# Kernel tuning notes

Measured on AMD Instinct MI355X. Metric: run time of the kernel, lower is better.

The kernel has to match this reference:

```python
import jax, jax.numpy as jnp
import numpy as np

B = 1000        # graphs in batch
T_PER = 250     # tasks per graph
M_PER = 50      # machines per graph
N_T = B * T_PER
N_M = B * M_PER
D_T = 16        # INPUT_TASK_DIM
D_M = 8         # INPUT_MACHINE_DIM
H = 128         # hidden_dim
IN_PREV_IDX = 0
TASK_FEAT_IDX = 1
EPS = 1e-5      # BatchNorm eps


def _mk_params(rng):
    def lin(i, o):
        return (rng.standard_normal((i, o)).astype(np.float32) / np.sqrt(i),
                np.zeros(o, np.float32))
    p = {}
    p['bn_t_gamma'] = np.ones(D_T, np.float32); p['bn_t_beta'] = np.zeros(D_T, np.float32)
    p['Wt1'], p['bt1'] = lin(D_T, H); p['Wt2'], p['bt2'] = lin(H, H)
    p['bn_m_gamma'] = np.ones(D_M, np.float32); p['bn_m_beta'] = np.zeros(D_M, np.float32)
    p['Wm1'], p['bm1'] = lin(D_M, H); p['Wm2'], p['bm2'] = lin(H, H)
    p['Wa1'], p['ba1'] = lin(2 * H, H); p['Wa2'], p['ba2'] = lin(H, H)
    p['Wl1'], p['bl1'] = lin(3 * H, H); p['Wl2'], p['bl2'] = lin(H, H)
    p['Wo1'], p['bo1'] = lin(H, H); p['Wo2'], p['bo2'] = lin(H, 1)
    return p


def setup_inputs() -> dict:
    rng = np.random.default_rng(0)
    xt = rng.standard_normal((N_T, D_T)).astype(np.float32)
    # prev-task flag: even task ids are 'prev'
    xt[:, IN_PREV_IDX] = (np.arange(N_T) % 2 == 0).astype(np.float32)
    # per-graph machine assignment in [0, M_PER), or -1 (unassigned) every 10th task
    lm = rng.integers(0, M_PER, N_T)
    lm[np.arange(N_T) % 10 == 0] = -1
    xt[:, TASK_FEAT_IDX] = lm.astype(np.float32)
    xm = rng.standard_normal((N_M, D_M)).astype(np.float32)
    inp = {'x_tasks': jnp.asarray(xt), 'x_machines': jnp.asarray(xm)}
    inp.update({k: jnp.asarray(v) for k, v in _mk_params(rng).items()})
    inp['x_tasks_batch'] = jnp.asarray(np.repeat(np.arange(B), T_PER).astype(np.int32))
    inp['x_machines_batch'] = jnp.asarray(np.repeat(np.arange(B), M_PER).astype(np.int32))
    # labels are tasks 0,5,10,...; prev tasks are even ids -> prev-local index t//2
    # label tasks that are prev: t % 10 == 0 -> prev_tasks_label_idx = 5*arange(N_T//10)
    inp['label_idx'] = jnp.asarray((5 * np.arange(N_T // 10)).astype(np.int32))
    inp['num_graphs'] = B
    return inp


def _bn(x, g, b):
    # BatchNorm1d in training mode: biased batch stats
    mu = x.mean(axis=0)
    var = x.var(axis=0)
    return g * (x - mu) * jax.lax.rsqrt(var + EPS) + b


def _seg_mean(x, seg, n):
    s = jax.ops.segment_sum(x, seg, num_segments=n)
    c = jax.ops.segment_sum(jnp.ones((x.shape[0], 1), x.dtype), seg, num_segments=n)
    return s / jnp.maximum(c, 1.0)


def reference(x_tasks, x_machines, bn_t_gamma, bn_t_beta, Wt1, bt1, Wt2, bt2,
              bn_m_gamma, bn_m_beta, Wm1, bm1, Wm2, bm2,
              Wa1, ba1, Wa2, ba2, Wl1, bl1, Wl2, bl2,
              Wo1, bo1, Wo2, bo2,
              x_tasks_batch, x_machines_batch, label_idx, num_graphs):
    nm = x_machines.shape[0]
    # tasks_select_assignment: local machine id -> global machine row (or pad row nm)
    tm_col = x_tasks[:, TASK_FEAT_IDX]
    cnt_m = jnp.bincount(x_machines_batch, length=num_graphs)
    cum = jnp.cumsum(cnt_m) - cnt_m  # cumulative machines per graph
    task_m = jnp.where(tm_col == -1.0, nm,
                       tm_col.astype(jnp.int32) + cum[x_tasks_batch].astype(jnp.int32))
    # node embeddings: BN -> Linear -> ReLU -> Linear -> ReLU
    th = jax.nn.relu(jax.nn.relu(_bn(x_tasks, bn_t_gamma, bn_t_beta) @ Wt1 + bt1) @ Wt2 + bt2)
    mh = jax.nn.relu(jax.nn.relu(_bn(x_machines, bn_m_gamma, bn_m_beta) @ Wm1 + bm1) @ Wm2 + bm2)
    # global aggregation per graph (scatter_mean) + MLP
    aggr = jnp.concatenate([_seg_mean(th, x_tasks_batch, num_graphs),
                            _seg_mean(mh, x_machines_batch, num_graphs)], axis=1)
    aggr = jax.nn.relu(aggr @ Wa1 + ba1) @ Wa2 + ba2
    # gather machine embedding per task (pad row of zeros for unassigned)
    mh_pad = jnp.concatenate([mh, jnp.zeros((1, H), mh.dtype)], axis=0)
    cat = jnp.concatenate([th, aggr[x_tasks_batch], mh_pad[task_m]], axis=1)  # [N_T, 3H]
    h = jax.nn.relu(cat @ Wl1 + bl1) @ Wl2 + bl2
    out = (jax.nn.relu(h @ Wo1 + bo1) @ Wo2 + bo2)[label_idx]
    return out
```

## Files before the change

### kernel.cpp

```cpp
#include <hip/hip_runtime.h>

constexpr int B     = 1000;
constexpr int T_PER = 250;
constexpr int M_PER = 50;
constexpr int N_T   = B * T_PER;
constexpr int N_M   = B * M_PER;
constexpr int H     = 128;
constexpr int N_LBL = 25000;
constexpr float EPS = 1e-05f;

constexpr int NB_T = 256;
constexpr int NB_M = 64;
constexpr int NB_P = 64;

constexpr int OFF_PART_T = 0;
constexpr int OFF_PART_M = OFF_PART_T + NB_T * 32;
constexpr int OFF_AT     = OFF_PART_M + NB_M * 16;
constexpr int OFF_BT     = OFF_AT + 16;
constexpr int OFF_AM     = OFF_BT + 16;
constexpr int OFF_BM     = OFF_AM + 8;
constexpr int OFF_BT1F   = OFF_BM + 8;
constexpr int OFF_BM1F   = OFF_BT1F + 128;
constexpr int OFF_MEANT  = OFF_BM1F + 128;
constexpr int OFF_MEANM  = OFF_MEANT + B * H;
constexpr int OFF_AGG2   = OFF_MEANM + B * H;
constexpr int OFF_HALF   = OFF_AGG2 + B * H;
constexpr int HO_WT1  = 0;
constexpr int HO_WT2  = 4096;
constexpr int HO_WM1  = 20480;
constexpr int HO_WM2  = 24576;
constexpr int HO_WA1  = 40960;
constexpr int HO_WA2  = 73728;
constexpr int HO_WL1  = 90112;
constexpr int HO_WL2  = 139264;
constexpr int HO_WO1  = 155648;
constexpr int HO_XT16 = 172032;
constexpr int HO_XM16 = HO_XT16 + N_T * 16;

typedef _Float16 f16x8 __attribute__((ext_vector_type(8)));
typedef _Float16 f16x4 __attribute__((ext_vector_type(4)));
typedef float f32x4 __attribute__((ext_vector_type(4)));

#define MFMA16(a, b, c) __builtin_amdgcn_mfma_f32_16x16x32_f16(a, b, c, 0, 0, 0)

template <int C, int NB>
__device__ __forceinline__ void stats_body(const float* __restrict__ x,
                                           _Float16* __restrict__ x16, int nelem,
                                           float* __restrict__ part, int blk, int t,
                                           float* ls, float* lq) {
    float s = 0.f, q = 0.f;
    for (int e = blk * 256 + t; e < nelem; e += NB * 256) {
        float v = x[e];
        s += v;
        q += v * v;
        x16[e] = (_Float16)v;
    }
    ls[t] = s; lq[t] = q;
    __syncthreads();
    if (t < C) {
        float S = 0.f, Q = 0.f;
        for (int u = t; u < 256; u += C) { S += ls[u]; Q += lq[u]; }
        part[blk * 2 * C + t] = S;
        part[blk * 2 * C + C + t] = Q;
    }
}

__device__ __forceinline__ void cvt_tr(const float* __restrict__ src, _Float16* __restrict__ dst,
                                       int K, int Kp, int tid, int nt) {
    for (int idx = tid; idx < 128 * Kp; idx += nt) {
        int c = idx / Kp, k = idx - c * Kp;
        float v = (k < K) ? src[k * 128 + c] : 0.f;
        dst[idx] = (_Float16)v;
    }
}

__global__ __launch_bounds__(256) void stats_prep_kernel(
        const float* __restrict__ xt, const float* __restrict__ xm,
        _Float16* __restrict__ xt16, _Float16* __restrict__ xm16,
        const float* __restrict__ Wt2, const float* __restrict__ Wm2,
        const float* __restrict__ Wa1, const float* __restrict__ Wa2,
        const float* __restrict__ Wl1, const float* __restrict__ Wl2,
        const float* __restrict__ Wo1,
        float* __restrict__ wsf, _Float16* __restrict__ wh) {
    __shared__ float ls[256], lq[256];
    const int bid = blockIdx.x, t = threadIdx.x;
    if (bid < NB_T) {
        stats_body<16, NB_T>(xt, xt16, N_T * 16, wsf + OFF_PART_T, bid, t, ls, lq);
    } else if (bid < NB_T + NB_M) {
        stats_body<8, NB_M>(xm, xm16, N_M * 8, wsf + OFF_PART_M, bid - NB_T, t, ls, lq);
    } else {
        const int tid = (bid - NB_T - NB_M) * 256 + t;
        const int nt = NB_P * 256;
        cvt_tr(Wt2, wh + HO_WT2, 128, 128, tid, nt);
        cvt_tr(Wm2, wh + HO_WM2, 128, 128, tid, nt);
        cvt_tr(Wa1, wh + HO_WA1, 256, 256, tid, nt);
        cvt_tr(Wa2, wh + HO_WA2, 128, 128, tid, nt);
        cvt_tr(Wl1, wh + HO_WL1, 384, 384, tid, nt);
        cvt_tr(Wl2, wh + HO_WL2, 128, 128, tid, nt);
        cvt_tr(Wo1, wh + HO_WO1, 128, 128, tid, nt);
    }
}

__global__ __launch_bounds__(256) void finalize_kernel(
        const float* __restrict__ gt, const float* __restrict__ btb,
        const float* __restrict__ gm, const float* __restrict__ bmb,
        const float* __restrict__ Wt1, const float* __restrict__ bt1,
        const float* __restrict__ Wm1, const float* __restrict__ bm1,
        float* __restrict__ ws, _Float16* __restrict__ wh) {
    __shared__ float red[256];
    __shared__ float statT[32], statM[16];
    __shared__ float shT[16], shM[8];
    __shared__ float saT[16], saM[8];
    const int t = threadIdx.x;
    {
        const int slot = t & 31, chunk = t >> 5;
        const float* p = ws + OFF_PART_T;
        float s = 0.f;
        for (int b = chunk * 32; b < chunk * 32 + 32; b++) s += p[b * 32 + slot];
        red[t] = s;
    }
    __syncthreads();
    if (t < 32) {
        float v = 0.f;
#pragma unroll
        for (int c = 0; c < 8; c++) v += red[t + 32 * c];
        statT[t] = v;
    }
    __syncthreads();
    {
        float s = 0.f;
        if (t < 128) {
            const int slot = t & 15, chunk = t >> 4;
            const float* p = ws + OFF_PART_M;
            for (int b = chunk * 8; b < chunk * 8 + 8; b++) s += p[b * 16 + slot];
        }
        red[t] = s;
    }
    __syncthreads();
    if (t < 16) {
        float v = 0.f;
#pragma unroll
        for (int c = 0; c < 8; c++) v += red[t + 16 * c];
        statM[t] = v;
    }
    __syncthreads();
    if (t < 16) {
        float mu  = statT[t] / (float)N_T;
        float var = statT[16 + t] / (float)N_T - mu * mu;
        float a   = gt[t] * rsqrtf(var + EPS);
        ws[OFF_AT + t] = a;
        float b = btb[t] - mu * a;
        ws[OFF_BT + t] = b;
        shT[t] = b;
        saT[t] = a;
    } else if (t < 24) {
        int c = t - 16;
        float mu  = statM[c] / (float)N_M;
        float var = statM[8 + c] / (float)N_M - mu * mu;
        float a   = gm[c] * rsqrtf(var + EPS);
        ws[OFF_AM + c] = a;
        float b = bmb[c] - mu * a;
        ws[OFF_BM + c] = b;
        shM[c] = b;
        saM[c] = a;
    }
    __syncthreads();
    if (t < 128) {
        float s = bt1[t];
#pragma unroll
        for (int k = 0; k < 16; k++) s += shT[k] * Wt1[k * 128 + t];
        ws[OFF_BT1F + t] = s;
        _Float16 row[32];
#pragma unroll
        for (int k = 0; k < 16; k++) row[k] = (_Float16)(Wt1[k * 128 + t] * saT[k]);
        float bh = (float)(_Float16)s;
        row[16] = (_Float16)s;
        row[17] = (_Float16)(s - bh);
#pragma unroll
        for (int k = 18; k < 32; k++) row[k] = (_Float16)0.f;
#pragma unroll
        for (int q = 0; q < 4; q++)
            *(f16x8*)(wh + HO_WT1 + t * 32 + q * 8) = *(const f16x8*)(row + q * 8);
    } else {
        int c = t - 128;
        float s = bm1[c];
#pragma unroll
        for (int k = 0; k < 8; k++) s += shM[k] * Wm1[k * 128 + c];
        ws[OFF_BM1F + c] = s;
        _Float16 row[32];
#pragma unroll
        for (int k = 0; k < 8; k++) row[k] = (_Float16)(Wm1[k * 128 + c] * saM[k]);
        float bh = (float)(_Float16)s;
        row[8] = (_Float16)s;
        row[9] = (_Float16)(s - bh);
#pragma unroll
        for (int k = 10; k < 32; k++) row[k] = (_Float16)0.f;
#pragma unroll
        for (int q = 0; q < 4; q++)
            *(f16x8*)(wh + HO_WM1 + c * 32 + q * 8) = *(const f16x8*)(row + q * 8);
    }
}

__device__ __forceinline__ void zacc(f32x4 acc[4][2]) {
#pragma unroll
    for (int rg = 0; rg < 4; rg++)
#pragma unroll
        for (int mi = 0; mi < 2; mi++) acc[rg][mi] = (f32x4){0.f, 0.f, 0.f, 0.f};
}

__device__ __forceinline__ void ld32(f16x8 w[2], const _Float16* __restrict__ WT,
                                     int m0, int r, int gq) {
#pragma unroll
    for (int mi = 0; mi < 2; mi++)
        w[mi] = *(const f16x8*)(WT + ((m0 + mi) * 16 + r) * 32 + gq * 8);
}

__device__ __forceinline__ void ld128(f16x8 w[2][4], const _Float16* __restrict__ WT,
                                      int lda, int k0, int m0, int r, int gq) {
#pragma unroll
    for (int mi = 0; mi < 2; mi++)
#pragma unroll
        for (int ks = 0; ks < 4; ks++)
            w[mi][ks] = *(const f16x8*)(WT + ((m0 + mi) * 16 + r) * lda + k0 + ks * 32 + gq * 8);
}

__device__ __forceinline__ void mm32g(const f16x8 w[2], const f16x8 xb[4], f32x4 acc[4][2]) {
#pragma unroll
    for (int rg = 0; rg < 4; rg++) {
        acc[rg][0] = MFMA16(w[0], xb[rg], acc[rg][0]);
        acc[rg][1] = MFMA16(w[1], xb[rg], acc[rg][1]);
    }
}

__device__ __forceinline__ void mm32(const f16x8 w[2], const _Float16* __restrict__ act,
                                     int rstride, int r, int gq, f32x4 acc[4][2]) {
#pragma unroll
    for (int rg = 0; rg < 4; rg++) {
        const f16x8 bf = *(const f16x8*)(act + (rg * 16 + r) * rstride + gq * 8);
        acc[rg][0] = MFMA16(w[0], bf, acc[rg][0]);
        acc[rg][1] = MFMA16(w[1], bf, acc[rg][1]);
    }
}

__device__ __forceinline__ void mm128(const f16x8 w[2][4], const _Float16* __restrict__ act,
                                      int rstride, int r, int gq, f32x4 acc[4][2]) {
#pragma unroll
    for (int rg = 0; rg < 4; rg++)
#pragma unroll
        for (int ks = 0; ks < 4; ks++) {
            const f16x8 bf = *(const f16x8*)(act + (rg * 16 + r) * rstride + ks * 32 + gq * 8);
            acc[rg][0] = MFMA16(w[0][ks], bf, acc[rg][0]);
            acc[rg][1] = MFMA16(w[1][ks], bf, acc[rg][1]);
        }
}

__device__ __forceinline__ void epi_cs(const f32x4 acc[4][2], const f32x4 bv[2],
                                       _Float16* __restrict__ dst, int dstride,
                                       int m0, int r, int gq, bool relu) {
#pragma unroll
    for (int rg = 0; rg < 4; rg++)
#pragma unroll
        for (int mi = 0; mi < 2; mi++) {
            f16x4 hv;
#pragma unroll
            for (int j = 0; j < 4; j++) {
                float v = acc[rg][mi][j] + bv[mi][j];
                if (relu) v = fmaxf(v, 0.f);
                hv[j] = (_Float16)v;
            }
            *(f16x4*)(dst + (rg * 16 + r) * dstride + (m0 + mi) * 16 + gq * 4) = hv;
        }
}

__global__ __launch_bounds__(256, 3) void seg_tile4(
        const _Float16* __restrict__ xt16, const _Float16* __restrict__ xm16,
        const _Float16* __restrict__ wh, const float* __restrict__ wsf,
        const float* __restrict__ bt2, const float* __restrict__ bm2,
        float* __restrict__ meanT, float* __restrict__ meanM) {
    __shared__ __attribute__((aligned(16))) _Float16 h1s[64 * 136];
    const int t = threadIdx.x, lane = t & 63, w = t >> 6;
    const int r = lane & 15, gq = lane >> 4;
    const int m0 = 2 * w;
    const bool taskb = (blockIdx.x < B);
    const _Float16* W1T = wh + (taskb ? HO_WT1 : HO_WM1);
    const _Float16* W2T = wh + (taskb ? HO_WT2 : HO_WM2);
    const float* b1f = wsf + (taskb ? OFF_BT1F : OFF_BM1F);
    const float* b2  = taskb ? bt2 : bm2;
    const _Float16* x16 = taskb ? xt16 : xm16;
    const int ROWS = taskb ? T_PER : M_PER;
    const int CIN  = taskb ? 16 : 8;
    f16x8 w1[2]; ld32(w1, W1T, m0, r, gq);
    f16x8 w2[2][4]; ld128(w2, W2T, 128, 0, m0, r, gq);
    f32x4 b1v[2], b2v[2];
#pragma unroll
    for (int mi = 0; mi < 2; mi++) {
        b1v[mi] = *(const f32x4*)(b1f + (m0 + mi) * 16 + gq * 4);
        b2v[mi] = *(const f32x4*)(b2 + (m0 + mi) * 16 + gq * 4);
    }
    f16x8 z8;
#pragma unroll
    for (int e = 0; e < 8; e++) z8[e] = (_Float16)0.f;
    const bool loader = taskb ? (gq < 2) : (gq == 0);
    const int gb = taskb ? blockIdx.x : 0;
    const int mg0 = taskb ? 0 : (blockIdx.x - B) * 4;
    const f32x4 zf = (f32x4){0.f, 0.f, 0.f, 0.f};
    f32x4 rs[2];
    rs[0] = zf; rs[1] = zf;
    f16x8 xb[4];
    {
        const int g0 = taskb ? gb : mg0;
#pragma unroll
        for (int rg = 0; rg < 4; rg++) {
            int row = rg * 16 + r;
            int cl = (row < ROWS) ? row : (ROWS - 1);
            xb[rg] = loader ? *(const f16x8*)(x16 + (g0 * ROWS + cl) * CIN + gq * 8) : z8;
        }
    }
    for (int it = 0; it < 4; it++) {
        const int g = taskb ? gb : (mg0 + it);
        const int rbase = taskb ? (it * 64) : 0;
        f32x4 acc[4][2];
        zacc(acc);
        mm32g(w1, xb, acc);
        epi_cs(acc, b1v, h1s, 136, m0, r, gq, true);
        __syncthreads();
        if (it < 3) {
            const int gn = taskb ? gb : (mg0 + it + 1);
            const int rbn = taskb ? ((it + 1) * 64) : 0;
#pragma unroll
            for (int rg = 0; rg < 4; rg++) {
                int row = rbn + rg * 16 + r;
                int cl = (row < ROWS) ? row : (ROWS - 1);
                xb[rg] = loader ? *(const f16x8*)(x16 + (gn * ROWS + cl) * CIN + gq * 8) : z8;
            }
        }
        zacc(acc);
        mm128(w2, h1s, 136, r, gq, acc);
        if (taskb) {
            if (rbase + 64 <= ROWS) {
#pragma unroll
                for (int rg = 0; rg < 4; rg++)
#pragma unroll
                    for (int mi = 0; mi < 2; mi++)
#pragma unroll
                        for (int j = 0; j < 4; j++)
                            rs[mi][j] += fmaxf(acc[rg][mi][j] + b2v[mi][j], 0.f);
            } else {
#pragma unroll
                for (int rg = 0; rg < 4; rg++) {
                    const float mk = ((rbase + rg * 16 + r) < ROWS) ? 1.f : 0.f;
#pragma unroll
                    for (int mi = 0; mi < 2; mi++)
#pragma unroll
                        for (int j = 0; j < 4; j++)
                            rs[mi][j] = fmaf(fmaxf(acc[rg][mi][j] + b2v[mi][j], 0.f), mk, rs[mi][j]);
                }
            }
        } else {
            f32x4 ms[2];
            ms[0] = zf; ms[1] = zf;
#pragma unroll
            for (int rg = 0; rg < 4; rg++) {
                const float mk = ((rg * 16 + r) < ROWS) ? 1.f : 0.f;
#pragma unroll
                for (int mi = 0; mi < 2; mi++)
#pragma unroll
                    for (int j = 0; j < 4; j++)
                        ms[mi][j] = fmaf(fmaxf(acc[rg][mi][j] + b2v[mi][j], 0.f), mk, ms[mi][j]);
            }
#pragma unroll
            for (int mi = 0; mi < 2; mi++)
#pragma unroll
                for (int j = 0; j < 4; j++) {
                    float v = ms[mi][j];
                    v += __shfl_xor(v, 1); v += __shfl_xor(v, 2);
                    v += __shfl_xor(v, 4); v += __shfl_xor(v, 8);
                    ms[mi][j] = v;
                }
            if (r == 0) {
                const float inv = 1.f / (float)M_PER;
#pragma unroll
                for (int mi = 0; mi < 2; mi++) {
                    f32x4 st = ms[mi] * inv;
                    *(f32x4*)(meanM + g * H + (m0 + mi) * 16 + gq * 4) = st;
                }
            }
        }
        if (it < 3) __syncthreads();
    }
    if (taskb) {
#pragma unroll
        for (int mi = 0; mi < 2; mi++)
#pragma unroll
            for (int j = 0; j < 4; j++) {
                float v = rs[mi][j];
                v += __shfl_xor(v, 1); v += __shfl_xor(v, 2);
                v += __shfl_xor(v, 4); v += __shfl_xor(v, 8);
                rs[mi][j] = v;
            }
        if (r == 0) {
            const float inv = 1.f / (float)T_PER;
#pragma unroll
            for (int mi = 0; mi < 2; mi++) {
                f32x4 st = rs[mi] * inv;
                *(f32x4*)(meanT + gb * H + (m0 + mi) * 16 + gq * 4) = st;
            }
        }
    }
}

__global__ __launch_bounds__(256) void aggr_kernel(const float* __restrict__ meanT, const float* __restrict__ meanM,
        const _Float16* __restrict__ Wa1T, const float* __restrict__ ba1,
        const _Float16* __restrict__ Wa2T, const float* __restrict__ ba2,
        const _Float16* __restrict__ Wl1T, const float* __restrict__ bl1,
        float* __restrict__ agg2) {
    __shared__ __attribute__((aligned(16))) _Float16 cin[16 * 264];
    __shared__ __attribute__((aligned(16))) _Float16 h1s[16 * 136];
    __shared__ __attribute__((aligned(16))) _Float16 ags[16 * 136];
    const int t = threadIdx.x, lane = t & 63, wave = t >> 6;
    const int r = lane & 15, gq = lane >> 4;
    const int m0 = 2 * wave;
    const int g0 = blockIdx.x * 16;
    f16x8 wa1[2][8], wa2[2][4], wl1b[2][4];
#pragma unroll
    for (int mi = 0; mi < 2; mi++)
#pragma unroll
        for (int ks = 0; ks < 8; ks++)
            wa1[mi][ks] = *(const f16x8*)(Wa1T + ((m0 + mi) * 16 + r) * 256 + ks * 32 + gq * 8);
    ld128(wa2, Wa2T, 128, 0, m0, r, gq);
    ld128(wl1b, Wl1T, 384, 128, m0, r, gq);
    f32x4 b1v[2], b2v[2], blv[2];
#pragma unroll
    for (int mi = 0; mi < 2; mi++) {
        b1v[mi] = *(const f32x4*)(ba1 + (m0 + mi) * 16 + gq * 4);
        b2v[mi] = *(const f32x4*)(ba2 + (m0 + mi) * 16 + gq * 4);
        blv[mi] = *(const f32x4*)(bl1 + (m0 + mi) * 16 + gq * 4);
    }
    for (int e = t; e < 16 * 64; e += 256) {
        int j = e >> 6, c4 = e & 63;
        int g = g0 + j;
        float4 v = {0.f, 0.f, 0.f, 0.f};
        if (g < B) v = (c4 < 32) ? *(const float4*)(meanT + g * H + c4 * 4)
                                 : *(const float4*)(meanM + g * H + (c4 - 32) * 4);
        f16x4 hv;
        hv[0] = (_Float16)v.x; hv[1] = (_Float16)v.y; hv[2] = (_Float16)v.z; hv[3] = (_Float16)v.w;
        *(f16x4*)(cin + j * 264 + c4 * 4) = hv;
    }
    __syncthreads();
    f32x4 a0 = {0.f, 0.f, 0.f, 0.f}, a1 = {0.f, 0.f, 0.f, 0.f};
    {
        const _Float16* bp = cin + r * 264 + gq * 8;
#pragma unroll
        for (int ks = 0; ks < 8; ks++) {
            const f16x8 bf = *(const f16x8*)(bp + ks * 32);
            a0 = MFMA16(wa1[0][ks], bf, a0);
            a1 = MFMA16(wa1[1][ks], bf, a1);
        }
    }
    {
        f16x4 h0, h1v;
#pragma unroll
        for (int j = 0; j < 4; j++) {
            h0[j]  = (_Float16)fmaxf(a0[j] + b1v[0][j], 0.f);
            h1v[j] = (_Float16)fmaxf(a1[j] + b1v[1][j], 0.f);
        }
        *(f16x4*)(h1s + r * 136 + m0 * 16 + gq * 4) = h0;
        *(f16x4*)(h1s + r * 136 + (m0 + 1) * 16 + gq * 4) = h1v;
    }
    __syncthreads();
    a0 = (f32x4){0.f, 0.f, 0.f, 0.f}; a1 = (f32x4){0.f, 0.f, 0.f, 0.f};
    {
        const _Float16* bp = h1s + r * 136 + gq * 8;
#pragma unroll
        for (int ks = 0; ks < 4; ks++) {
            const f16x8 bf = *(const f16x8*)(bp + ks * 32);
            a0 = MFMA16(wa2[0][ks], bf, a0);
            a1 = MFMA16(wa2[1][ks], bf, a1);
        }
    }
    {
        f16x4 h0, h1v;
#pragma unroll
        for (int j = 0; j < 4; j++) {
            h0[j]  = (_Float16)(a0[j] + b2v[0][j]);
            h1v[j] = (_Float16)(a1[j] + b2v[1][j]);
        }
        *(f16x4*)(ags + r * 136 + m0 * 16 + gq * 4) = h0;
        *(f16x4*)(ags + r * 136 + (m0 + 1) * 16 + gq * 4) = h1v;
    }
    __syncthreads();
    a0 = (f32x4){0.f, 0.f, 0.f, 0.f}; a1 = (f32x4){0.f, 0.f, 0.f, 0.f};
    {
        const _Float16* bp = ags + r * 136 + gq * 8;
#pragma unroll
        for (int ks = 0; ks < 4; ks++) {
            const f16x8 bf = *(const f16x8*)(bp + ks * 32);
            a0 = MFMA16(wl1b[0][ks], bf, a0);
            a1 = MFMA16(wl1b[1][ks], bf, a1);
        }
    }
    if (g0 + r < B) {
        *(f32x4*)(agg2 + (g0 + r) * H + m0 * 16 + gq * 4) = a0 + blv[0];
        *(f32x4*)(agg2 + (g0 + r) * H + (m0 + 1) * 16 + gq * 4) = a1 + blv[1];
    }
}

__global__ __launch_bounds__(256) void label_kernel(
        const float* __restrict__ xt,
        const _Float16* __restrict__ xt16, const _Float16* __restrict__ xm16,
        const _Float16* __restrict__ Wt1T, const float* __restrict__ bt1f,
        const _Float16* __restrict__ Wt2T, const float* __restrict__ bt2,
        const _Float16* __restrict__ Wm1T, const float* __restrict__ bm1f,
        const _Float16* __restrict__ Wm2T, const float* __restrict__ bm2,
        const _Float16* __restrict__ Wl1T,
        const _Float16* __restrict__ Wl2T, const float* __restrict__ bl2,
        const _Float16* __restrict__ Wo1T, const float* __restrict__ bo1,
        const float* __restrict__ Wo2, const float* __restrict__ bo2,
        const float* __restrict__ agg2,
        const int* __restrict__ tbatch, const int* __restrict__ lidx,
        float* __restrict__ out) {
    __shared__ __attribute__((aligned(16))) _Float16 xs_t[64 * 40];
    __shared__ __attribute__((aligned(16))) _Float16 xs_m[64 * 40];
    __shared__ __attribute__((aligned(16))) _Float16 h1s[64 * 136];
    __shared__ __attribute__((aligned(16))) _Float16 cat[64 * 264];
    __shared__ float psum[4][64];
    __shared__ int ridx[64], gidx[64], midx[64];
    const int t = threadIdx.x;
    const int lane = t & 63, wave = t >> 6;
    const int r = lane & 15, gq = lane >> 4;
    const int m0 = 2 * wave;
    if (t < 64) {
        int i = blockIdx.x * 64 + t;
        int rr = (i < N_LBL) ? lidx[i] : 0;
        ridx[t] = rr;
        int gg = tbatch[rr];
        gidx[t] = gg;
        float tv = xt[rr * 16 + 1];
        midx[t] = (tv == -1.0f) ? -1 : ((int)tv + gg * M_PER);
    }
    __syncthreads();
    f16x4 z4; z4[0] = z4[1] = z4[2] = z4[3] = (_Float16)0.f;
    {
        int j = t >> 2, part = t & 3;
        f16x4 hv = *(const f16x4*)(xt16 + ridx[j] * 16 + part * 4);
        *(f16x4*)(xs_t + j * 40 + part * 4) = hv;
        *(f16x4*)(xs_t + j * 40 + 16 + part * 4) = z4;
    }
    if (t < 128) {
        int j = t >> 1, part = t & 1;
        int m = midx[j];
        f16x4 hv = z4;
        if (m >= 0) hv = *(const f16x4*)(xm16 + m * 8 + part * 4);
        *(f16x4*)(xs_m + j * 40 + part * 4) = hv;
#pragma unroll
        for (int q = 0; q < 3; q++)
            *(f16x4*)(xs_m + j * 40 + 8 + part * 12 + q * 4) = z4;
    }
    __syncthreads();
    f32x4 agg2v[4][2];
#pragma unroll
    for (int rg = 0; rg < 4; rg++)
#pragma unroll
        for (int mi = 0; mi < 2; mi++)
            agg2v[rg][mi] = *(const f32x4*)(agg2 + gidx[rg * 16 + r] * H + (m0 + mi) * 16 + gq * 4);
    f32x4 acc[4][2];
    f16x8 wt1[2]; ld32(wt1, Wt1T, m0, r, gq);
    f16x8 wt2[2][4]; ld128(wt2, Wt2T, 128, 0, m0, r, gq);
    f32x4 bva[2], bvb[2];
#pragma unroll
    for (int mi = 0; mi < 2; mi++) {
        bva[mi] = *(const f32x4*)(bt1f + (m0 + mi) * 16 + gq * 4);
        bvb[mi] = *(const f32x4*)(bt2 + (m0 + mi) * 16 + gq * 4);
    }
    zacc(acc);
    mm32(wt1, xs_t, 40, r, gq, acc);
    epi_cs(acc, bva, h1s, 136, m0, r, gq, true);
    f16x8 wm1[2]; ld32(wm1, Wm1T, m0, r, gq);
    __syncthreads();
    zacc(acc);
    mm128(wt2, h1s, 136, r, gq, acc);
    epi_cs(acc, bvb, cat, 264, m0, r, gq, true);
    f16x8 wm2[2][4]; ld128(wm2, Wm2T, 128, 0, m0, r, gq);
    __syncthreads();
#pragma unroll
    for (int mi = 0; mi < 2; mi++) {
        bva[mi] = *(const f32x4*)(bm1f + (m0 + mi) * 16 + gq * 4);
        bvb[mi] = *(const f32x4*)(bm2 + (m0 + mi) * 16 + gq * 4);
    }
    zacc(acc);
    mm32(wm1, xs_m, 40, r, gq, acc);
    epi_cs(acc, bva, h1s, 136, m0, r, gq, true);
    f16x8 wl1a[2][4]; ld128(wl1a, Wl1T, 384, 0, m0, r, gq);
    __syncthreads();
    zacc(acc);
    mm128(wm2, h1s, 136, r, gq, acc);
#pragma unroll
    for (int rg = 0; rg < 4; rg++) {
        const bool sent = (midx[rg * 16 + r] < 0);
#pragma unroll
        for (int mi = 0; mi < 2; mi++) {
            f16x4 hv;
#pragma unroll
            for (int j = 0; j < 4; j++) {
                float v = fmaxf(acc[rg][mi][j] + bvb[mi][j], 0.f);
                hv[j] = (_Float16)(sent ? 0.f : v);
            }
            *(f16x4*)(cat + (rg * 16 + r) * 264 + 128 + (m0 + mi) * 16 + gq * 4) = hv;
        }
    }
    f16x8 wl1c[2][4]; ld128(wl1c, Wl1T, 384, 256, m0, r, gq);
    __syncthreads();
    zacc(acc);
    mm128(wl1a, cat, 264, r, gq, acc);
    mm128(wl1c, cat + 128, 264, r, gq, acc);
#pragma unroll
    for (int rg = 0; rg < 4; rg++)
#pragma unroll
        for (int mi = 0; mi < 2; mi++) {
            f16x4 hv;
#pragma unroll
            for (int j = 0; j < 4; j++)
                hv[j] = (_Float16)fmaxf(acc[rg][mi][j] + agg2v[rg][mi][j], 0.f);
            *(f16x4*)(h1s + (rg * 16 + r) * 136 + (m0 + mi) * 16 + gq * 4) = hv;
        }
    f16x8 wl2[2][4]; ld128(wl2, Wl2T, 128, 0, m0, r, gq);
    __syncthreads();
#pragma unroll
    for (int mi = 0; mi < 2; mi++) bva[mi] = *(const f32x4*)(bl2 + (m0 + mi) * 16 + gq * 4);
    zacc(acc);
    mm128(wl2, h1s, 136, r, gq, acc);
    epi_cs(acc, bva, cat, 264, m0, r, gq, false);
    f16x8 wo1[2][4]; ld128(wo1, Wo1T, 128, 0, m0, r, gq);
    __syncthreads();
#pragma unroll
    for (int mi = 0; mi < 2; mi++) bva[mi] = *(const f32x4*)(bo1 + (m0 + mi) * 16 + gq * 4);
    f32x4 wo2v[2];
#pragma unroll
    for (int mi = 0; mi < 2; mi++) wo2v[mi] = *(const f32x4*)(Wo2 + (m0 + mi) * 16 + gq * 4);
    zacc(acc);
    mm128(wo1, cat, 264, r, gq, acc);
#pragma unroll
    for (int rg = 0; rg < 4; rg++) {
        float pv = 0.f;
#pragma unroll
        for (int mi = 0; mi < 2; mi++)
#pragma unroll
            for (int j = 0; j < 4; j++)
                pv += fmaxf(acc[rg][mi][j] + bva[mi][j], 0.f) * wo2v[mi][j];
        pv += __shfl_xor(pv, 16);
        pv += __shfl_xor(pv, 32);
        if (lane < 16) psum[wave][rg * 16 + lane] = pv;
    }
    __syncthreads();
    if (t < 64) {
        int i = blockIdx.x * 64 + t;
        if (i < N_LBL)
            out[i] = psum[0][t] + psum[1][t] + psum[2][t] + psum[3][t] + bo2[0];
    }
}

extern "C" void kernel_launch(void* const* d_in, const int* in_sizes, int n_in,
                              void* d_out, int out_size, void* d_ws, size_t ws_size,
                              hipStream_t stream) {
    const float* xt  = (const float*)d_in[0];
    const float* xm  = (const float*)d_in[1];
    const float* gt  = (const float*)d_in[2];
    const float* btb = (const float*)d_in[3];
    const float* Wt1 = (const float*)d_in[4];  const float* bt1 = (const float*)d_in[5];
    const float* Wt2 = (const float*)d_in[6];  const float* bt2 = (const float*)d_in[7];
    const float* gm  = (const float*)d_in[8];  const float* bmb = (const float*)d_in[9];
    const float* Wm1 = (const float*)d_in[10]; const float* bm1 = (const float*)d_in[11];
    const float* Wm2 = (const float*)d_in[12]; const float* bm2 = (const float*)d_in[13];
    const float* Wa1 = (const float*)d_in[14]; const float* ba1 = (const float*)d_in[15];
    const float* Wa2 = (const float*)d_in[16]; const float* ba2 = (const float*)d_in[17];
    const float* Wl1 = (const float*)d_in[18]; const float* bl1 = (const float*)d_in[19];
    const float* Wl2 = (const float*)d_in[20]; const float* bl2 = (const float*)d_in[21];
    const float* Wo1 = (const float*)d_in[22]; const float* bo1 = (const float*)d_in[23];
    const float* Wo2 = (const float*)d_in[24]; const float* bo2 = (const float*)d_in[25];
    const int* tb  = (const int*)d_in[26];
    const int* lix = (const int*)d_in[28];
    float* wsf = (float*)d_ws;
    _Float16* wh = (_Float16*)(wsf + OFF_HALF);
    _Float16* xt16 = wh + HO_XT16;
    _Float16* xm16 = wh + HO_XM16;
    float* outp = (float*)d_out;

    stats_prep_kernel<<<NB_T + NB_M + NB_P, 256, 0, stream>>>(
        xt, xm, xt16, xm16, Wt2, Wm2, Wa1, Wa2, Wl1, Wl2, Wo1, wsf, wh);
    finalize_kernel<<<1, 256, 0, stream>>>(gt, btb, gm, bmb, Wt1, bt1, Wm1, bm1, wsf, wh);
    seg_tile4<<<B + 250, 256, 0, stream>>>(xt16, xm16, wh, wsf, bt2, bm2,
                                           wsf + OFF_MEANT, wsf + OFF_MEANM);
    aggr_kernel<<<(B + 15) / 16, 256, 0, stream>>>(wsf + OFF_MEANT, wsf + OFF_MEANM,
                                                   wh + HO_WA1, ba1, wh + HO_WA2, ba2,
                                                   wh + HO_WL1, bl1, wsf + OFF_AGG2);
    label_kernel<<<(N_LBL + 63) / 64, 256, 0, stream>>>(xt, xt16, xm16,
                                                        wh + HO_WT1, wsf + OFF_BT1F, wh + HO_WT2, bt2,
                                                        wh + HO_WM1, wsf + OFF_BM1F, wh + HO_WM2, bm2,
                                                        wh + HO_WL1,
                                                        wh + HO_WL2, bl2,
                                                        wh + HO_WO1, bo1, Wo2, bo2,
                                                        wsf + OFF_AGG2, tb, lix, outp);
}
```

Measured before the change: 73.11 us.

## Fold Wl2 and Wo1 into one precomputed weight matrix with fused bias

Because no nonlinearity sits between the Wl2 and Wo1 linear layers, the two are algebraically combined into a single 128x128 matrix Wl2·Wo1 with bias bl2·Wo1+bo1. The combined weights are computed in fp16 MFMA inside the single-block finalize kernel. The label kernel therefore does one GEMM and one barrier fewer per tile and skips writing the intermediate back to shared memory. In exchange, the finalize kernel (one block, which also uses the prep kernel's Wo1 conversion) takes longer, and fp16 rounding of the fused product changes numerics slightly.

```diff
diff --git a/kernel.cpp b/kernel.cpp
--- a/kernel.cpp
+++ b/kernel.cpp
@@ -24,7 +24,8 @@
 constexpr int OFF_MEANT  = OFF_BM1F + 128;
 constexpr int OFF_MEANM  = OFF_MEANT + B * H;
 constexpr int OFF_AGG2   = OFF_MEANM + B * H;
-constexpr int OFF_HALF   = OFF_AGG2 + B * H;
+constexpr int OFF_BFOLD  = OFF_AGG2 + B * H;
+constexpr int OFF_HALF   = OFF_BFOLD + 128;
 constexpr int HO_WT1  = 0;
 constexpr int HO_WT2  = 4096;
 constexpr int HO_WM1  = 20480;
@@ -32,7 +33,7 @@
 constexpr int HO_WA1  = 40960;
 constexpr int HO_WA2  = 73728;
 constexpr int HO_WL1  = 90112;
-constexpr int HO_WL2  = 139264;
+constexpr int HO_WLO  = 139264;
 constexpr int HO_WO1  = 155648;
 constexpr int HO_XT16 = 172032;
 constexpr int HO_XM16 = HO_XT16 + N_T * 16;
@@ -42,6 +43,77 @@
 typedef float f32x4 __attribute__((ext_vector_type(4)));
 
 #define MFMA16(a, b, c) __builtin_amdgcn_mfma_f32_16x16x32_f16(a, b, c, 0, 0, 0)
+
+__device__ __forceinline__ void zacc(f32x4 acc[4][2]) {
+#pragma unroll
+    for (int rg = 0; rg < 4; rg++)
+#pragma unroll
+        for (int mi = 0; mi < 2; mi++) acc[rg][mi] = (f32x4){0.f, 0.f, 0.f, 0.f};
+}
+
+__device__ __forceinline__ void ld32(f16x8 w[2], const _Float16* __restrict__ WT,
+                                     int m0, int r, int gq) {
+#pragma unroll
+    for (int mi = 0; mi < 2; mi++)
+        w[mi] = *(const f16x8*)(WT + ((m0 + mi) * 16 + r) * 32 + gq * 8);
+}
+
+__device__ __forceinline__ void ld128(f16x8 w[2][4], const _Float16* __restrict__ WT,
+                                      int lda, int k0, int m0, int r, int gq) {
+#pragma unroll
+    for (int mi = 0; mi < 2; mi++)
+#pragma unroll
+        for (int ks = 0; ks < 4; ks++)
+            w[mi][ks] = *(const f16x8*)(WT + ((m0 + mi) * 16 + r) * lda + k0 + ks * 32 + gq * 8);
+}
+
+__device__ __forceinline__ void mm32g(const f16x8 w[2], const f16x8 xb[4], f32x4 acc[4][2]) {
+#pragma unroll
+    for (int rg = 0; rg < 4; rg++) {
+        acc[rg][0] = MFMA16(w[0], xb[rg], acc[rg][0]);
+        acc[rg][1] = MFMA16(w[1], xb[rg], acc[rg][1]);
+    }
+}
+
+__device__ __forceinline__ void mm32(const f16x8 w[2], const _Float16* __restrict__ act,
+                                     int rstride, int r, int gq, f32x4 acc[4][2]) {
+#pragma unroll
+    for (int rg = 0; rg < 4; rg++) {
+        const f16x8 bf = *(const f16x8*)(act + (rg * 16 + r) * rstride + gq * 8);
+        acc[rg][0] = MFMA16(w[0], bf, acc[rg][0]);
+        acc[rg][1] = MFMA16(w[1], bf, acc[rg][1]);
+    }
+}
+
+__device__ __forceinline__ void mm128(const f16x8 w[2][4], const _Float16* __restrict__ act,
+                                      int rstride, int r, int gq, f32x4 acc[4][2]) {
+#pragma unroll
+    for (int rg = 0; rg < 4; rg++)
+#pragma unroll
+        for (int ks = 0; ks < 4; ks++) {
+            const f16x8 bf = *(const f16x8*)(act + (rg * 16 + r) * rstride + ks * 32 + gq * 8);
+            acc[rg][0] = MFMA16(w[0][ks], bf, acc[rg][0]);
+            acc[rg][1] = MFMA16(w[1][ks], bf, acc[rg][1]);
+        }
+}
+
+__device__ __forceinline__ void epi_cs(const f32x4 acc[4][2], const f32x4 bv[2],
+                                       _Float16* __restrict__ dst, int dstride,
+                                       int m0, int r, int gq, bool relu) {
+#pragma unroll
+    for (int rg = 0; rg < 4; rg++)
+#pragma unroll
+        for (int mi = 0; mi < 2; mi++) {
+            f16x4 hv;
+#pragma unroll
+            for (int j = 0; j < 4; j++) {
+                float v = acc[rg][mi][j] + bv[mi][j];
+                if (relu) v = fmaxf(v, 0.f);
+                hv[j] = (_Float16)v;
+            }
+            *(f16x4*)(dst + (rg * 16 + r) * dstride + (m0 + mi) * 16 + gq * 4) = hv;
+        }
+}
 
 template <int C, int NB>
 __device__ __forceinline__ void stats_body(const float* __restrict__ x,
@@ -79,8 +151,7 @@
         _Float16* __restrict__ xt16, _Float16* __restrict__ xm16,
         const float* __restrict__ Wt2, const float* __restrict__ Wm2,
         const float* __restrict__ Wa1, const float* __restrict__ Wa2,
-        const float* __restrict__ Wl1, const float* __restrict__ Wl2,
-        const float* __restrict__ Wo1,
+        const float* __restrict__ Wl1, const float* __restrict__ Wo1,
         float* __restrict__ wsf, _Float16* __restrict__ wh) {
     __shared__ float ls[256], lq[256];
     const int bid = blockIdx.x, t = threadIdx.x;
@@ -96,7 +167,6 @@
         cvt_tr(Wa1, wh + HO_WA1, 256, 256, tid, nt);
         cvt_tr(Wa2, wh + HO_WA2, 128, 128, tid, nt);
         cvt_tr(Wl1, wh + HO_WL1, 384, 384, tid, nt);
-        cvt_tr(Wl2, wh + HO_WL2, 128, 128, tid, nt);
         cvt_tr(Wo1, wh + HO_WO1, 128, 128, tid, nt);
     }
 }
@@ -106,11 +176,14 @@
         const float* __restrict__ gm, const float* __restrict__ bmb,
         const float* __restrict__ Wt1, const float* __restrict__ bt1,
         const float* __restrict__ Wm1, const float* __restrict__ bm1,
+        const float* __restrict__ Wl2, const float* __restrict__ bl2,
+        const float* __restrict__ Wo1, const float* __restrict__ bo1,
         float* __restrict__ ws, _Float16* __restrict__ wh) {
     __shared__ float red[256];
     __shared__ float statT[32], statM[16];
     __shared__ float shT[16], shM[8];
     __shared__ float saT[16], saM[8];
+    __shared__ __attribute__((aligned(16))) _Float16 tlo[128 * 136];
     const int t = threadIdx.x;
     {
         const int slot = t & 31, chunk = t >> 5;
@@ -199,77 +272,62 @@
         for (int q = 0; q < 4; q++)
             *(f16x8*)(wh + HO_WM1 + c * 32 + q * 8) = *(const f16x8*)(row + q * 8);
     }
-}
-
-__device__ __forceinline__ void zacc(f32x4 acc[4][2]) {
-#pragma unroll
-    for (int rg = 0; rg < 4; rg++)
-#pragma unroll
-        for (int mi = 0; mi < 2; mi++) acc[rg][mi] = (f32x4){0.f, 0.f, 0.f, 0.f};
-}
-
-__device__ __forceinline__ void ld32(f16x8 w[2], const _Float16* __restrict__ WT,
-                                     int m0, int r, int gq) {
-#pragma unroll
-    for (int mi = 0; mi < 2; mi++)
-        w[mi] = *(const f16x8*)(WT + ((m0 + mi) * 16 + r) * 32 + gq * 8);
-}
-
-__device__ __forceinline__ void ld128(f16x8 w[2][4], const _Float16* __restrict__ WT,
-                                      int lda, int k0, int m0, int r, int gq) {
-#pragma unroll
-    for (int mi = 0; mi < 2; mi++)
-#pragma unroll
-        for (int ks = 0; ks < 4; ks++)
-            w[mi][ks] = *(const f16x8*)(WT + ((m0 + mi) * 16 + r) * lda + k0 + ks * 32 + gq * 8);
-}
-
-__device__ __forceinline__ void mm32g(const f16x8 w[2], const f16x8 xb[4], f32x4 acc[4][2]) {
-#pragma unroll
-    for (int rg = 0; rg < 4; rg++) {
-        acc[rg][0] = MFMA16(w[0], xb[rg], acc[rg][0]);
-        acc[rg][1] = MFMA16(w[1], xb[rg], acc[rg][1]);
-    }
-}
-
-__device__ __forceinline__ void mm32(const f16x8 w[2], const _Float16* __restrict__ act,
-                                     int rstride, int r, int gq, f32x4 acc[4][2]) {
-#pragma unroll
-    for (int rg = 0; rg < 4; rg++) {
-        const f16x8 bf = *(const f16x8*)(act + (rg * 16 + r) * rstride + gq * 8);
-        acc[rg][0] = MFMA16(w[0], bf, acc[rg][0]);
-        acc[rg][1] = MFMA16(w[1], bf, acc[rg][1]);
-    }
-}
-
-__device__ __forceinline__ void mm128(const f16x8 w[2][4], const _Float16* __restrict__ act,
-                                      int rstride, int r, int gq, f32x4 acc[4][2]) {
-#pragma unroll
-    for (int rg = 0; rg < 4; rg++)
-#pragma unroll
-        for (int ks = 0; ks < 4; ks++) {
-            const f16x8 bf = *(const f16x8*)(act + (rg * 16 + r) * rstride + ks * 32 + gq * 8);
-            acc[rg][0] = MFMA16(w[0][ks], bf, acc[rg][0]);
-            acc[rg][1] = MFMA16(w[1][ks], bf, acc[rg][1]);
-        }
-}
-
-__device__ __forceinline__ void epi_cs(const f32x4 acc[4][2], const f32x4 bv[2],
-                                       _Float16* __restrict__ dst, int dstride,
-                                       int m0, int r, int gq, bool relu) {
-#pragma unroll
-    for (int rg = 0; rg < 4; rg++)
-#pragma unroll
-        for (int mi = 0; mi < 2; mi++) {
-            f16x4 hv;
-#pragma unroll
-            for (int j = 0; j < 4; j++) {
-                float v = acc[rg][mi][j] + bv[mi][j];
-                if (relu) v = fmaxf(v, 0.f);
-                hv[j] = (_Float16)v;
-            }
-            *(f16x4*)(dst + (rg * 16 + r) * dstride + (m0 + mi) * 16 + gq * 4) = hv;
-        }
+    {
+        const int lane = t & 63, wv = t >> 6;
+        const int r = lane & 15, gq = lane >> 4;
+        const int m0 = 2 * wv;
+        f16x8 wo1f[2][4];
+        ld128(wo1f, wh + HO_WO1, 128, 0, m0, r, gq);
+#pragma unroll
+        for (int half = 0; half < 2; half++) {
+            f32x4 acc[4][2];
+            zacc(acc);
+#pragma unroll
+            for (int rg = 0; rg < 4; rg++) {
+                const int k = half * 64 + rg * 16 + r;
+#pragma unroll
+                for (int ks = 0; ks < 4; ks++) {
+                    const float* src = Wl2 + k * 128 + ks * 32 + gq * 8;
+                    float4 a = *(const float4*)(src);
+                    float4 b = *(const float4*)(src + 4);
+                    f16x8 bf;
+                    bf[0] = (_Float16)a.x; bf[1] = (_Float16)a.y;
+                    bf[2] = (_Float16)a.z; bf[3] = (_Float16)a.w;
+                    bf[4] = (_Float16)b.x; bf[5] = (_Float16)b.y;
+                    bf[6] = (_Float16)b.z; bf[7] = (_Float16)b.w;
+                    acc[rg][0] = MFMA16(wo1f[0][ks], bf, acc[rg][0]);
+                    acc[rg][1] = MFMA16(wo1f[1][ks], bf, acc[rg][1]);
+                }
+            }
+#pragma unroll
+            for (int rg = 0; rg < 4; rg++) {
+                const int k = half * 64 + rg * 16 + r;
+#pragma unroll
+                for (int mi = 0; mi < 2; mi++) {
+                    f16x4 hv;
+#pragma unroll
+                    for (int j = 0; j < 4; j++) hv[j] = (_Float16)acc[rg][mi][j];
+                    *(f16x4*)(tlo + k * 136 + (m0 + mi) * 16 + gq * 4) = hv;
+                }
+            }
+        }
+    }
+    __syncthreads();
+    {
+        const int o = t >> 1, kh = (t & 1) * 64;
+#pragma unroll
+        for (int q = 0; q < 8; q++) {
+            _Float16 buf[8];
+#pragma unroll
+            for (int e = 0; e < 8; e++) buf[e] = tlo[(kh + q * 8 + e) * 136 + o];
+            *(f16x8*)(wh + HO_WLO + o * 128 + kh + q * 8) = *(const f16x8*)buf;
+        }
+    }
+    if (t < 128) {
+        float s = bo1[t];
+        for (int k = 0; k < 128; k++) s += bl2[k] * Wo1[k * 128 + t];
+        ws[OFF_BFOLD + t] = s;
+    }
 }
 
 __global__ __launch_bounds__(256, 3) void seg_tile4(
@@ -513,8 +571,7 @@
         const _Float16* __restrict__ Wm1T, const float* __restrict__ bm1f,
         const _Float16* __restrict__ Wm2T, const float* __restrict__ bm2,
         const _Float16* __restrict__ Wl1T,
-        const _Float16* __restrict__ Wl2T, const float* __restrict__ bl2,
-        const _Float16* __restrict__ Wo1T, const float* __restrict__ bo1,
+        const _Float16* __restrict__ WloT, const float* __restrict__ bfold,
         const float* __restrict__ Wo2, const float* __restrict__ bo2,
         const float* __restrict__ agg2,
         const int* __restrict__ tbatch, const int* __restrict__ lidx,
@@ -623,22 +680,15 @@
                 hv[j] = (_Float16)fmaxf(acc[rg][mi][j] + agg2v[rg][mi][j], 0.f);
             *(f16x4*)(h1s + (rg * 16 + r) * 136 + (m0 + mi) * 16 + gq * 4) = hv;
         }
-    f16x8 wl2[2][4]; ld128(wl2, Wl2T, 128, 0, m0, r, gq);
-    __syncthreads();
-#pragma unroll
-    for (int mi = 0; mi < 2; mi++) bva[mi] = *(const f32x4*)(bl2 + (m0 + mi) * 16 + gq * 4);
-    zacc(acc);
-    mm128(wl2, h1s, 136, r, gq, acc);
-    epi_cs(acc, bva, cat, 264, m0, r, gq, false);
-    f16x8 wo1[2][4]; ld128(wo1, Wo1T, 128, 0, m0, r, gq);
-    __syncthreads();
-#pragma unroll
-    for (int mi = 0; mi < 2; mi++) bva[mi] = *(const f32x4*)(bo1 + (m0 + mi) * 16 + gq * 4);
+    f16x8 wlo[2][4]; ld128(wlo, WloT, 128, 0, m0, r, gq);
+    __syncthreads();
+#pragma unroll
+    for (int mi = 0; mi < 2; mi++) bva[mi] = *(const f32x4*)(bfold + (m0 + mi) * 16 + gq * 4);
     f32x4 wo2v[2];
 #pragma unroll
     for (int mi = 0; mi < 2; mi++) wo2v[mi] = *(const f32x4*)(Wo2 + (m0 + mi) * 16 + gq * 4);
     zacc(acc);
-    mm128(wo1, cat, 264, r, gq, acc);
+    mm128(wlo, h1s, 136, r, gq, acc);
 #pragma unroll
     for (int rg = 0; rg < 4; rg++) {
         float pv = 0.f;
@@ -686,8 +736,9 @@
     float* outp = (float*)d_out;
 
     stats_prep_kernel<<<NB_T + NB_M + NB_P, 256, 0, stream>>>(
-        xt, xm, xt16, xm16, Wt2, Wm2, Wa1, Wa2, Wl1, Wl2, Wo1, wsf, wh);
-    finalize_kernel<<<1, 256, 0, stream>>>(gt, btb, gm, bmb, Wt1, bt1, Wm1, bm1, wsf, wh);
+        xt, xm, xt16, xm16, Wt2, Wm2, Wa1, Wa2, Wl1, Wo1, wsf, wh);
+    finalize_kernel<<<1, 256, 0, stream>>>(gt, btb, gm, bmb, Wt1, bt1, Wm1, bm1,
+                                           Wl2, bl2, Wo1, bo1, wsf, wh);
     seg_tile4<<<B + 250, 256, 0, stream>>>(xt16, xm16, wh, wsf, bt2, bm2,
                                            wsf + OFF_MEANT, wsf + OFF_MEANM);
     aggr_kernel<<<(B + 15) / 16, 256, 0, stream>>>(wsf + OFF_MEANT, wsf + OFF_MEANM,
@@ -697,7 +748,7 @@
                                                         wh + HO_WT1, wsf + OFF_BT1F, wh + HO_WT2, bt2,
                                                         wh + HO_WM1, wsf + OFF_BM1F, wh + HO_WM2, bm2,
                                                         wh + HO_WL1,
-                                                        wh + HO_WL2, bl2,
-                                                        wh + HO_WO1, bo1, Wo2, bo2,
+                                                        wh + HO_WLO, wsf + OFF_BFOLD,
+                                                        Wo2, bo2,
                                                         wsf + OFF_AGG2, tb, lix, outp);
 }
```

Result: slower. 87.28 us (+19.4%).
